# Performance work log

Hardware: AMD Instinct MI355X
Metric: run time of the kernel (lower is better)

## Reference

```python
import jax, jax.numpy as jnp
import numpy as np

DIM = 1024
N_HEADS = 16
HEAD_DIM = DIM // N_HEADS
SCALE = HEAD_DIM ** -0.5


def setup_inputs() -> dict:
    key = jax.random.key(0)
    kx, kq, kk, kv = jax.random.split(key, 4)
    x = jax.random.normal(kx, (2, 2048, DIM), dtype=jnp.float32)
    bv_q = jax.random.normal(kq, (N_HEADS, HEAD_DIM), dtype=jnp.float32) * 0.02
    bv_k = jax.random.normal(kk, (N_HEADS, HEAD_DIM), dtype=jnp.float32) * 0.02
    bv_v = jax.random.normal(kv, (N_HEADS, HEAD_DIM), dtype=jnp.float32) * 0.02
    return {"x": x, "bv_q": bv_q, "bv_k": bv_k, "bv_v": bv_v}


def reference(x, bv_q, bv_k, bv_v):
    B, T, D = x.shape
    H, HD = N_HEADS, HEAD_DIM
    x_h = x.reshape(B, T, H, HD)
    # sign-gated Q/K/V (sign of binding vectors; elementwise +/-1 gating)
    Q = x_h * jnp.sign(bv_q)  # [B,T,H,HD]
    K = x_h * jnp.sign(bv_k)
    V = x_h * jnp.sign(bv_v)
    # causal scores, sigmoid gating (no softmax)
    scores = jnp.einsum('bqhd,bkhd->bhqk', Q, K) * SCALE  # [B,H,T,T]
    causal = jnp.tril(jnp.ones((T, T), dtype=bool))
    attn = jnp.where(causal, jax.nn.sigmoid(scores * 4.0), 0.0)
    out = jnp.einsum('bhqk,bkhd->bqhd', attn, V)  # [B,T,H,HD]
    return out.reshape(B, T, D)
```

## Files before the change

kernel.cpp:

```cpp
#include <hip/hip_runtime.h>
#include <hip/hip_bf16.h>
#include <stdint.h>

#define DIM 1024
#define T_LEN 2048
#define NB 2
#define NH 16
#define HD 64
#define NQT 32

typedef float f32x4 __attribute__((ext_vector_type(4)));
typedef float f32x16 __attribute__((ext_vector_type(16)));
typedef __bf16 bf16x8 __attribute__((ext_vector_type(8)));
typedef __bf16 bf16x2 __attribute__((ext_vector_type(2)));
typedef unsigned int u32;
typedef unsigned int u32x4 __attribute__((ext_vector_type(4)));

__device__ __forceinline__ float sgnf(float v) {
    return (v > 0.f) ? 1.f : ((v < 0.f) ? -1.f : 0.f);
}

__device__ __forceinline__ float sigmoid_half(float v) {
    return __builtin_amdgcn_rcpf(1.f + __builtin_amdgcn_exp2f(-0.72134752f * v));
}

__device__ __forceinline__ u32 pack2(float p0, float p1) {
    bf16x2 t = {(__bf16)p0, (__bf16)p1};
    return __builtin_bit_cast(u32, t);
}

__device__ __forceinline__ void gload16(const __bf16* g, __bf16* l) {
    __builtin_amdgcn_global_load_lds(
        (__attribute__((address_space(1))) void*)g,
        (__attribute__((address_space(3))) void*)l,
        16, 0, 0);
}

__global__ __launch_bounds__(256) void prep_kernel(
    const float* __restrict__ x, __bf16* __restrict__ xb, __bf16* __restrict__ xt)
{
    __shared__ __align__(16) __bf16 tile[64][72];

    const int bid = blockIdx.x;
    const int h = bid & 15, tmp = bid >> 4, tt = tmp & 31, b = tmp >> 5;
    const int tid = threadIdx.x;
    const int r = tid >> 2, c0 = (tid & 3) * 16;

    const size_t rowbase = ((size_t)(b * T_LEN + tt * 64 + r)) * DIM + h * HD + c0;
    const float* xp = x + rowbase;

    __bf16 v[16];
    #pragma unroll
    for (int i = 0; i < 16; i += 4) {
        f32x4 f = *(const f32x4*)(xp + i);
        #pragma unroll
        for (int j = 0; j < 4; ++j) v[i + j] = (__bf16)f[j];
    }
    bf16x8 s0, s1;
    #pragma unroll
    for (int j = 0; j < 8; ++j) { s0[j] = v[j]; s1[j] = v[8 + j]; }
    *(bf16x8*)(xb + rowbase)     = s0;
    *(bf16x8*)(xb + rowbase + 8) = s1;
    *(bf16x8*)&tile[r][c0]     = s0;
    *(bf16x8*)&tile[r][c0 + 8] = s1;

    __syncthreads();

    const int d = tid >> 2, t0c = (tid & 3) * 16;
    __bf16 ov[16];
    #pragma unroll
    for (int i = 0; i < 16; ++i) ov[i] = tile[t0c + i][d];
    bf16x8 o0, o1;
    #pragma unroll
    for (int j = 0; j < 8; ++j) { o0[j] = ov[j]; o1[j] = ov[8 + j]; }
    const size_t obase = ((size_t)((b * NH + h) * HD + d)) * T_LEN + tt * 64 + t0c;
    *(bf16x8*)(xt + obase)     = o0;
    *(bf16x8*)(xt + obase + 8) = o1;
}

__global__ __launch_bounds__(256, 3) void mba_main(
    const __bf16* __restrict__ xb, const __bf16* __restrict__ xt,
    const float* __restrict__ bvq, const float* __restrict__ bvk,
    const float* __restrict__ bvv, float* __restrict__ out)
{
    __shared__ __align__(16) __bf16 Kb[3][64][64];
    __shared__ __align__(16) __bf16 Vb[3][64][64];

    const int bid = blockIdx.x;
    const int qt = (NQT - 1) - (bid >> 5);
    const int bh = bid & 31;
    const int b = bh >> 4, h = bh & 15;
    const int q0 = qt * 64;

    const int tid = threadIdx.x;
    const int w = tid >> 6, l = tid & 63;
    const int c = l & 31, hi = l >> 5;
    const int qh = w & 1, sh = w >> 1;

    const size_t xb_bh = (size_t)b * T_LEN * DIM + h * HD;
    const size_t xt_bh = (size_t)((b * NH + h) * HD) * T_LEN;

    const int rr = l >> 3;
    const int sw = ((l & 7) ^ rr) << 3;

    auto STAGE = [&](int buf, int kvt) {
        const int kv0 = kvt * 64;
        #pragma unroll
        for (int pt = 0; pt < 2; ++pt) {
            const int r0 = w * 8 + pt * 32;
            gload16(xb + xb_bh + (size_t)(kv0 + r0 + rr) * DIM + sw, &Kb[buf][r0][0]);
            gload16(xt + xt_bh + (size_t)(r0 + rr) * T_LEN + kv0 + sw, &Vb[buf][r0][0]);
        }
    };

    STAGE(0, 0);
    if (qt >= 1) STAGE(1, 1);

    bf16x8 qa[4];
    {
        const float* bq = bvq + h * HD;
        const float* bk = bvk + h * HD;
        const int qrow = q0 + qh * 32 + c;
        #pragma unroll
        for (int m = 0; m < 4; ++m) {
            const int d0 = m * 16 + hi * 8;
            bf16x8 va = *(const bf16x8*)(xb + xb_bh + (size_t)qrow * DIM + d0);
            #pragma unroll
            for (int j = 0; j < 8; ++j) {
                float f = sgnf(bq[d0 + j]) * sgnf(bk[d0 + j]);
                qa[m][j] = (__bf16)((float)va[j] * f);
            }
        }
    }
    float sv[2];
    #pragma unroll
    for (int nd = 0; nd < 2; ++nd) sv[nd] = sgnf(bvv[h * HD + nd * 32 + c]);

    f32x16 o[2];
    #pragma unroll
    for (int nd = 0; nd < 2; ++nd)
        #pragma unroll
        for (int i = 0; i < 16; ++i) o[nd][i] = 0.f;

    int cur = 0;
    const int krow = sh * 32 + c;
    const int swz = (c & 7) << 4;

    for (int t = 0; t <= qt; ++t) {
        const bool last = (t == qt);
        if (last) { asm volatile("s_waitcnt vmcnt(0)" ::: "memory"); }
        else      { asm volatile("s_waitcnt vmcnt(4)" ::: "memory"); }
        __builtin_amdgcn_sched_barrier(0);
        __builtin_amdgcn_s_barrier();
        __builtin_amdgcn_sched_barrier(0);

        if (t + 2 <= qt) {
            int stg = cur + 2; if (stg >= 3) stg -= 3;
            STAGE(stg, t + 2);
        }

        f32x16 ss;
        #pragma unroll
        for (int i = 0; i < 16; ++i) ss[i] = 0.f;
        #pragma unroll
        for (int m = 0; m < 4; ++m) {
            bf16x8 kf = *(const bf16x8*)((const char*)&Kb[cur][krow][0]
                          + ((m * 32 + hi * 16) ^ swz));
            ss = __builtin_amdgcn_mfma_f32_32x32x16_bf16(kf, qa[m], ss, 0, 0, 0);
        }

        u32 W[8];
        #pragma unroll
        for (int i = 0; i < 8; ++i) {
            const int r0 = 2 * i;
            const int sl = (r0 & 3) + 8 * (r0 >> 2) + 4 * hi;
            float p0 = sigmoid_half(ss[r0]);
            float p1 = sigmoid_half(ss[r0 + 1]);
            if (last) {
                const int sg = sh * 32 + sl;
                const int qg = qh * 32 + c;
                if (sg > qg)     p0 = 0.f;
                if (sg + 1 > qg) p1 = 0.f;
            }
            W[i] = pack2(p0, p1);
        }

        asm volatile("v_permlane32_swap_b32 %0, %1" : "+v"(W[0]), "+v"(W[2]));
        asm volatile("v_permlane32_swap_b32 %0, %1" : "+v"(W[1]), "+v"(W[3]));
        asm volatile("v_permlane32_swap_b32 %0, %1" : "+v"(W[4]), "+v"(W[6]));
        asm volatile("v_permlane32_swap_b32 %0, %1" : "+v"(W[5]), "+v"(W[7]));
        bf16x8 pa[2];
        pa[0] = __builtin_bit_cast(bf16x8, (u32x4){W[0], W[1], W[2], W[3]});
        pa[1] = __builtin_bit_cast(bf16x8, (u32x4){W[4], W[5], W[6], W[7]});

        #pragma unroll
        for (int m = 0; m < 2; ++m) {
            #pragma unroll
            for (int nd = 0; nd < 2; ++nd) {
                bf16x8 vf = *(const bf16x8*)((const char*)&Vb[cur][nd * 32 + c][0]
                              + ((sh * 64 + m * 32 + hi * 16) ^ swz));
                o[nd] = __builtin_amdgcn_mfma_f32_32x32x16_bf16(pa[m], vf, o[nd], 0, 0, 0);
            }
        }
        cur = (cur == 2) ? 0 : cur + 1;
    }

    __syncthreads();
    float (*osc)[64] = (float(*)[64]) & Kb[0][0][0];

    if (sh == 1) {
        #pragma unroll
        for (int r = 0; r < 16; ++r) {
            const int qloc = (r & 3) + 8 * (r >> 2) + 4 * hi;
            #pragma unroll
            for (int nd = 0; nd < 2; ++nd)
                osc[qh * 32 + qloc][nd * 32 + c] = o[nd][r];
        }
    }
    __syncthreads();
    if (sh == 0) {
        #pragma unroll
        for (int r = 0; r < 16; ++r) {
            const int qloc = (r & 3) + 8 * (r >> 2) + 4 * hi;
            const size_t row = (size_t)(b * T_LEN + q0 + qh * 32 + qloc) * DIM + h * HD;
            #pragma unroll
            for (int nd = 0; nd < 2; ++nd) {
                float val = (o[nd][r] + osc[qh * 32 + qloc][nd * 32 + c]) * sv[nd];
                out[row + nd * 32 + c] = val;
            }
        }
    }
}

__global__ __launch_bounds__(256) void mba_fallback(
    const float* __restrict__ x,
    const float* __restrict__ bvq,
    const float* __restrict__ bvk,
    const float* __restrict__ bvv,
    float* __restrict__ out)
{
    __shared__ __align__(16) __bf16 Kb[64][72];
    __shared__ __align__(16) __bf16 Vt[HD][72];
    __shared__ __align__(16) __bf16 Pb[4][16][72];

    const int bid = blockIdx.x;
    const int qt  = (NQT - 1) - (bid & (NQT - 1));
    const int bh  = bid >> 5;
    const int b   = bh >> 4;
    const int h   = bh & 15;

    const int tid = threadIdx.x;
    const int w   = tid >> 6;
    const int l   = tid & 63;
    const int lq  = l & 15;
    const int lh  = l >> 4;

    const int  q0    = qt * 64;
    const long xbase = ((long)b * T_LEN) * DIM + h * HD;

    bf16x8 qa[2];
    {
        const int   qrow = q0 + w * 16 + lq;
        const float* qp  = x + xbase + (long)qrow * DIM + lh * 8;
        const float* gp  = bvq + h * HD + lh * 8;
        #pragma unroll
        for (int ks = 0; ks < 2; ++ks)
            #pragma unroll
            for (int j = 0; j < 8; ++j)
                qa[ks][j] = (__bf16)(qp[ks * 32 + j] * sgnf(gp[ks * 32 + j]));
    }

    f32x4 o[4];
    #pragma unroll
    for (int n = 0; n < 4; ++n) o[n] = (f32x4){0.f, 0.f, 0.f, 0.f};

    const int r_st = tid >> 2;
    const int c0   = (tid & 3) * 16;
    const float* gk = bvk + h * HD + c0;
    const float* gv = bvv + h * HD + c0;

    for (int kvt = 0; kvt <= qt; ++kvt) {
        const int kv0 = kvt * 64;
        __syncthreads();
        {
            const float* kp = x + xbase + (long)(kv0 + r_st) * DIM + c0;
            __bf16 kb[16];
            #pragma unroll
            for (int i = 0; i < 16; ++i) kb[i] = (__bf16)(kp[i] * sgnf(gk[i]));
            *(bf16x8*)&Kb[r_st][c0]     = *(bf16x8*)&kb[0];
            *(bf16x8*)&Kb[r_st][c0 + 8] = *(bf16x8*)&kb[8];
            #pragma unroll
            for (int i = 0; i < 16; ++i)
                Vt[c0 + i][r_st] = (__bf16)(kp[i] * sgnf(gv[i]));
        }
        __syncthreads();

        f32x4 s[4];
        #pragma unroll
        for (int n = 0; n < 4; ++n) s[n] = (f32x4){0.f, 0.f, 0.f, 0.f};
        #pragma unroll
        for (int ks = 0; ks < 2; ++ks)
            #pragma unroll
            for (int n = 0; n < 4; ++n) {
                bf16x8 kf = *(const bf16x8*)&Kb[n * 16 + lq][ks * 32 + lh * 8];
                s[n] = __builtin_amdgcn_mfma_f32_16x16x32_bf16(qa[ks], kf, s[n], 0, 0, 0);
            }

        const bool diag = (kvt == qt);
        #pragma unroll
        for (int n = 0; n < 4; ++n)
            #pragma unroll
            for (int j = 0; j < 4; ++j) {
                float p = sigmoid_half(s[n][j]);
                if (diag && (n * 16 + lq) > (w * 16 + lh * 4 + j)) p = 0.f;
                Pb[w][lh * 4 + j][n * 16 + lq] = (__bf16)p;
            }

        #pragma unroll
        for (int ks = 0; ks < 2; ++ks) {
            bf16x8 pf = *(const bf16x8*)&Pb[w][lq][ks * 32 + lh * 8];
            #pragma unroll
            for (int n = 0; n < 4; ++n) {
                bf16x8 vf = *(const bf16x8*)&Vt[n * 16 + lq][ks * 32 + lh * 8];
                o[n] = __builtin_amdgcn_mfma_f32_16x16x32_bf16(pf, vf, o[n], 0, 0, 0);
            }
        }
    }

    float* op = out + ((long)b * T_LEN + q0 + w * 16) * DIM + h * HD;
    #pragma unroll
    for (int n = 0; n < 4; ++n)
        #pragma unroll
        for (int j = 0; j < 4; ++j)
            op[(long)(lh * 4 + j) * DIM + n * 16 + lq] = o[n][j];
}

extern "C" void kernel_launch(void* const* d_in, const int* in_sizes, int n_in,
                              void* d_out, int out_size, void* d_ws, size_t ws_size,
                              hipStream_t stream) {
    (void)in_sizes; (void)n_in; (void)out_size;
    const float* x   = (const float*)d_in[0];
    const float* bvq = (const float*)d_in[1];
    const float* bvk = (const float*)d_in[2];
    const float* bvv = (const float*)d_in[3];
    float* out = (float*)d_out;

    const size_t XB_BYTES = (size_t)NB * T_LEN * DIM * sizeof(__bf16);
    const size_t XT_BYTES = XB_BYTES;

    if (ws_size < XB_BYTES + XT_BYTES) {
        mba_fallback<<<NB * NH * NQT, 256, 0, stream>>>(x, bvq, bvk, bvv, out);
        return;
    }

    __bf16* xb = (__bf16*)d_ws;
    __bf16* xt = xb + (size_t)NB * T_LEN * DIM;

    prep_kernel<<<NB * NQT * NH, 256, 0, stream>>>(x, xb, xt);
    mba_main<<<NB * NH * NQT, 256, 0, stream>>>(xb, xt, bvq, bvk, bvv, out);
}
```

Baseline: 47.80 us.

## Stage V one tile ahead with double buffer, raise occupancy, reorder q-tiles

Splits the K/V staging so K stays triple-buffered two tiles ahead while V is double-buffered and loaded only one tile ahead. This cuts LDS use per block so launch bounds can request four blocks per SIMD instead of three. Block-to-q-tile mapping changes from strictly descending to a serpentine order within groups of eight, to balance the causal workload across concurrently running blocks. The shorter V prefetch distance gives less latency hiding for V loads, and the register cap may cause spills.

```diff
diff --git a/kernel.cpp b/kernel.cpp
--- a/kernel.cpp
+++ b/kernel.cpp
@@ -78,16 +78,18 @@
     *(bf16x8*)(xt + obase + 8) = o1;
 }
 
-__global__ __launch_bounds__(256, 3) void mba_main(
+__global__ __launch_bounds__(256, 4) void mba_main(
     const __bf16* __restrict__ xb, const __bf16* __restrict__ xt,
     const float* __restrict__ bvq, const float* __restrict__ bvk,
     const float* __restrict__ bvv, float* __restrict__ out)
 {
     __shared__ __align__(16) __bf16 Kb[3][64][64];
-    __shared__ __align__(16) __bf16 Vb[3][64][64];
+    __shared__ __align__(16) __bf16 Vb[2][64][64];
 
     const int bid = blockIdx.x;
-    const int qt = (NQT - 1) - (bid >> 5);
+    const int u = bid >> 5;
+    const int jj = u >> 3, aa = u & 7;
+    const int qt = 8 * jj + ((jj & 1) ? (7 - aa) : aa);
     const int bh = bid & 31;
     const int b = bh >> 4, h = bh & 15;
     const int q0 = qt * 64;
@@ -103,18 +105,26 @@
     const int rr = l >> 3;
     const int sw = ((l & 7) ^ rr) << 3;
 
-    auto STAGE = [&](int buf, int kvt) {
-        const int kv0 = kvt * 64;
+    auto STAGE_K = [&](int buf, int kvt) {
+        const int kv0s = kvt * 64;
         #pragma unroll
         for (int pt = 0; pt < 2; ++pt) {
             const int r0 = w * 8 + pt * 32;
-            gload16(xb + xb_bh + (size_t)(kv0 + r0 + rr) * DIM + sw, &Kb[buf][r0][0]);
-            gload16(xt + xt_bh + (size_t)(r0 + rr) * T_LEN + kv0 + sw, &Vb[buf][r0][0]);
+            gload16(xb + xb_bh + (size_t)(kv0s + r0 + rr) * DIM + sw, &Kb[buf][r0][0]);
         }
     };
-
-    STAGE(0, 0);
-    if (qt >= 1) STAGE(1, 1);
+    auto STAGE_V = [&](int buf, int kvt) {
+        const int kv0s = kvt * 64;
+        #pragma unroll
+        for (int pt = 0; pt < 2; ++pt) {
+            const int r0 = w * 8 + pt * 32;
+            gload16(xt + xt_bh + (size_t)(r0 + rr) * T_LEN + kv0s + sw, &Vb[buf][r0][0]);
+        }
+    };
+
+    STAGE_K(0, 0);
+    STAGE_V(0, 0);
+    if (qt >= 1) STAGE_K(1, 1);
 
     bf16x8 qa[4];
     {
@@ -149,15 +159,18 @@
     for (int t = 0; t <= qt; ++t) {
         const bool last = (t == qt);
         if (last) { asm volatile("s_waitcnt vmcnt(0)" ::: "memory"); }
-        else      { asm volatile("s_waitcnt vmcnt(4)" ::: "memory"); }
+        else      { asm volatile("s_waitcnt vmcnt(2)" ::: "memory"); }
         __builtin_amdgcn_sched_barrier(0);
         __builtin_amdgcn_s_barrier();
         __builtin_amdgcn_sched_barrier(0);
 
+        if (t + 1 <= qt) STAGE_V((t + 1) & 1, t + 1);
+        __builtin_amdgcn_sched_barrier(0);
         if (t + 2 <= qt) {
             int stg = cur + 2; if (stg >= 3) stg -= 3;
-            STAGE(stg, t + 2);
-        }
+            STAGE_K(stg, t + 2);
+        }
+        __builtin_amdgcn_sched_barrier(0);
 
         f32x16 ss;
         #pragma unroll
@@ -197,7 +210,7 @@
         for (int m = 0; m < 2; ++m) {
             #pragma unroll
             for (int nd = 0; nd < 2; ++nd) {
-                bf16x8 vf = *(const bf16x8*)((const char*)&Vb[cur][nd * 32 + c][0]
+                bf16x8 vf = *(const bf16x8*)((const char*)&Vb[t & 1][nd * 32 + c][0]
                               + ((sh * 64 + m * 32 + hi * 16) ^ swz));
                 o[nd] = __builtin_amdgcn_mfma_f32_32x32x16_bf16(pa[m], vf, o[nd], 0, 0, 0);
             }
```

Result: no change. 47.43 us (-0.8%).
